# Optimization experiments

Measured on AMD Instinct MI355X. Metric: run time of the kernel, lower is better.

The kernel has to match this reference:

```python
import jax, jax.numpy as jnp
import numpy as np

N, K, P = 40000, 32, 15
C = 128            # output_feature_dim (kpconv in/out channels)
H_POS, D_POS = 64, 256
H_AGG, D_PROC = 256, 256
RADIUS = 1.0
KP_EXTENT = RADIUS / (P ** (1.0 / 3.0) - 1.0) * 1.5
SLOPE = 0.01       # nn.LeakyReLU default
EPS = 1e-5         # BatchNorm1d default eps


def _lin(key, din, dout):
    k1, k2 = jax.random.split(key)
    lim = 1.0 / np.sqrt(din)
    w = jax.random.uniform(k1, (din, dout), minval=-lim, maxval=lim, dtype=jnp.float32)
    b = jax.random.uniform(k2, (dout,), minval=-lim, maxval=lim, dtype=jnp.float32)
    return w, b


def _bn(x, g, b):
    # BatchNorm1d in training mode: biased batch statistics
    m = jnp.mean(x, axis=0)
    v = jnp.var(x, axis=0)
    return (x - m) * jax.lax.rsqrt(v + EPS) * g + b


def _lrelu(x):
    return jnp.where(x >= 0, x, SLOPE * x)


def setup_inputs() -> dict:
    key = jax.random.key(0)
    ks = jax.random.split(key, 16)
    inp = {}
    inp['points'] = jax.random.normal(ks[0], (N, 3), dtype=jnp.float32) * 10.0
    inp['covariances'] = jax.random.normal(ks[1], (N, 9), dtype=jnp.float32)
    inp['neighbors_index'] = jax.random.randint(ks[2], (N, K), 0, N)
    inp['pre_w'], inp['pre_b'] = _lin(ks[3], 9, C)
    inp['pre_bn_g'] = jnp.ones((C,), jnp.float32); inp['pre_bn_b'] = jnp.zeros((C,), jnp.float32)
    kp = jax.random.normal(ks[4], (P, 3), dtype=jnp.float32)
    kp = kp / jnp.linalg.norm(kp, axis=1, keepdims=True)
    inp['kernel_points'] = kp * jax.random.uniform(ks[5], (P, 1), dtype=jnp.float32) * RADIUS
    inp['kp_weights'] = jax.random.normal(ks[6], (P, C, C), dtype=jnp.float32) * (1.0 / np.sqrt(P * C))
    inp['pos_w1'], inp['pos_b1'] = _lin(ks[7], 3, H_POS)
    inp['pos_bn1_g'] = jnp.ones((H_POS,), jnp.float32); inp['pos_bn1_b'] = jnp.zeros((H_POS,), jnp.float32)
    inp['pos_w2'], inp['pos_b2'] = _lin(ks[8], H_POS, D_POS)
    inp['pos_bn2_g'] = jnp.ones((D_POS,), jnp.float32); inp['pos_bn2_b'] = jnp.zeros((D_POS,), jnp.float32)
    inp['agg_w1'], inp['agg_b1'] = _lin(ks[9], C, H_AGG)
    inp['agg_bn1_g'] = jnp.ones((H_AGG,), jnp.float32); inp['agg_bn1_b'] = jnp.zeros((H_AGG,), jnp.float32)
    inp['agg_w2'], inp['agg_b2'] = _lin(ks[10], H_AGG, D_PROC)
    inp['agg_bn2_g'] = jnp.ones((D_PROC,), jnp.float32); inp['agg_bn2_b'] = jnp.zeros((D_PROC,), jnp.float32)
    inp['keep_w1'], inp['keep_b1'] = _lin(ks[11], D_PROC, D_PROC // 4)
    inp['keep_bn_g'] = jnp.ones((D_PROC // 4,), jnp.float32); inp['keep_bn_b'] = jnp.zeros((D_PROC // 4,), jnp.float32)
    inp['keep_w2'], inp['keep_b2'] = _lin(ks[12], D_PROC // 4, 1)
    du = D_PROC + D_POS
    inp['uniq_w1'], inp['uniq_b1'] = _lin(ks[13], du, du // 4)
    inp['uniq_bn_g'] = jnp.ones((du // 4,), jnp.float32); inp['uniq_bn_b'] = jnp.zeros((du // 4,), jnp.float32)
    inp['uniq_w2'], inp['uniq_b2'] = _lin(ks[14], du // 4, 1)
    return inp


def reference(points, covariances, neighbors_index,
              pre_w, pre_b, pre_bn_g, pre_bn_b,
              kernel_points, kp_weights,
              pos_w1, pos_b1, pos_bn1_g, pos_bn1_b,
              pos_w2, pos_b2, pos_bn2_g, pos_bn2_b,
              agg_w1, agg_b1, agg_bn1_g, agg_bn1_b,
              agg_w2, agg_b2, agg_bn2_g, agg_bn2_b,
              keep_w1, keep_b1, keep_bn_g, keep_bn_b, keep_w2, keep_b2,
              uniq_w1, uniq_b1, uniq_bn_g, uniq_bn_b, uniq_w2, uniq_b2):
    # preactivation on 9-dim flattened covariances
    features = _lrelu(_bn(covariances @ pre_w + pre_b, pre_bn_g, pre_bn_b))  # [N, C]

    # ---- rigid KPConv (linear influence, sum aggregation, shadow point at index N) ----
    s_pad = jnp.concatenate([points, jnp.full((1, 3), 1e6, points.dtype)], axis=0)
    x_pad = jnp.concatenate([features, jnp.zeros((1, C), features.dtype)], axis=0)
    nb = s_pad[neighbors_index] - points[:, None, :]                          # [N, K, 3]
    # squared distances to kernel points without materializing [N,K,P,3]
    sq = (jnp.sum(nb * nb, -1)[:, :, None]
          + jnp.sum(kernel_points * kernel_points, -1)[None, None, :]
          - 2.0 * jnp.einsum('nkd,pd->nkp', nb, kernel_points))               # [N, K, P]
    infl = jnp.maximum(1.0 - jnp.sqrt(jnp.maximum(sq, 0.0)) / KP_EXTENT, 0.0)  # [N, K, P]
    nx = x_pad[neighbors_index]                                               # [N, K, C]
    weighted = jnp.einsum('nkp,nkc->npc', infl, nx)                           # [N, P, C]
    conv = jnp.einsum('npc,pcd->nd', weighted, kp_weights)                    # [N, C]
    # density normalization: count non-shadow neighbors
    nnum = jnp.maximum(jnp.sum(jnp.sum(nx, -1) > 0.0, axis=-1), 1)
    kpconv_feature = conv / nnum[:, None].astype(conv.dtype)

    # position embedding MLP
    pos = _lrelu(_bn(points @ pos_w1 + pos_b1, pos_bn1_g, pos_bn1_b))
    pos = _lrelu(_bn(pos @ pos_w2 + pos_b2, pos_bn2_g, pos_bn2_b))            # [N, 256]

    # feature aggregation MLP
    agg = _lrelu(_bn(kpconv_feature @ agg_w1 + agg_b1, agg_bn1_g, agg_bn1_b))
    agg = _lrelu(_bn(agg @ agg_w2 + agg_b2, agg_bn2_g, agg_bn2_b))            # [N, 256]

    # heads
    kh = _lrelu(_bn(agg @ keep_w1 + keep_b1, keep_bn_g, keep_bn_b))
    match_score = jax.nn.sigmoid((kh @ keep_w2 + keep_b2).ravel())
    u_in = jnp.concatenate([pos, agg], axis=1)                                # [N, 512]
    uh = _lrelu(_bn(u_in @ uniq_w1 + uniq_b1, uniq_bn_g, uniq_bn_b))
    unique_score = jax.nn.sigmoid((uh @ uniq_w2 + uniq_b2).ravel())
    return match_score, unique_score, neighbors_index
```

## Files before the change

### kernel.cpp

```cpp
#include <hip/hip_runtime.h>
#include <math.h>


#define NPTS 40000
#define KNB  32
#define PKP  15
#define SLOPE 0.01f
#define BNEPS 1e-5f
#define INV_N (1.0f/40000.0f)

typedef __attribute__((ext_vector_type(8))) short bf16x8;
typedef __attribute__((ext_vector_type(4))) float f32x4;

__device__ __forceinline__ float lrelu(float x){ return x >= 0.0f ? x : SLOPE*x; }
__device__ __forceinline__ unsigned short f2bf(float f){
  unsigned int b = __float_as_uint(f);
  b += 0x7fffu + ((b>>16)&1u);
  return (unsigned short)(b>>16);
}
__device__ __forceinline__ float bf2f(unsigned short u){
  return __uint_as_float(((unsigned int)u)<<16);
}


__global__ __launch_bounds__(256) void k_wprep_all(
    const float* __restrict__ kpw,  const float* __restrict__ pw2,
    const float* __restrict__ aw1,  const float* __restrict__ aw2,
    const float* __restrict__ kw1,  const float* __restrict__ uw1,
    unsigned short* __restrict__ wT){
  int i = blockIdx.x*256 + threadIdx.x;
  const float* src; int K, N, off, li;
  if      (i < 245760){ src=kpw; K=1920; N=128; off=0;      li=i; }
  else if (i < 262144){ src=pw2; K=64;   N=256; off=245760; li=i-245760; }
  else if (i < 294912){ src=aw1; K=128;  N=256; off=262144; li=i-262144; }
  else if (i < 360448){ src=aw2; K=256;  N=256; off=294912; li=i-294912; }
  else if (i < 376832){ src=kw1; K=256;  N=64;  off=360448; li=i-360448; }
  else                { src=uw1; K=512;  N=128; off=376832; li=i-376832; }
  int k = li / N, n = li - k*N;
  wT[(size_t)off + (size_t)n*K + k] = f2bf(src[li]);
}

__global__ __launch_bounds__(256) void k_moments(
    const float* __restrict__ cov, const float* __restrict__ pts,
    float* __restrict__ mom){
  int tid = threadIdx.x;
  int lane = tid & 63;
  int wv = (blockIdx.x*256 + tid) >> 6;
  int nw = gridDim.x*4;
  int kind = -1, ia = 0, ib = 0;
  if (lane < 9){ kind = 0; ia = lane; }
  else if (lane < 54){ int t = lane-9; int i = 0; while (t >= 9-i){ t -= 9-i; ++i; } kind = 1; ia = i; ib = i+t; }
  else if (lane < 57){ kind = 2; ia = lane-54; }
  else if (lane < 63){ int t = lane-57; int i = 0; while (t >= 3-i){ t -= 3-i; ++i; } kind = 3; ia = i; ib = i+t; }
  float part = 0.0f;
  for (int n = wv; n < NPTS; n += nw){
    float v = 0.0f;
    if (kind == 0) v = cov[n*9+ia];
    else if (kind == 1) v = cov[n*9+ia]*cov[n*9+ib];
    else if (kind == 2) v = pts[n*3+ia];
    else if (kind == 3) v = pts[n*3+ia]*pts[n*3+ib];
    part += v;
  }
  if (kind >= 0) atomicAdd(&mom[lane], part);
}

__global__ __launch_bounds__(256) void k_bnsetup(
    const float* __restrict__ preW, const float* __restrict__ preB,
    const float* __restrict__ preG, const float* __restrict__ preBB,
    const float* __restrict__ posW1, const float* __restrict__ posB1,
    const float* __restrict__ posG1, const float* __restrict__ posBB1,
    float* __restrict__ stats){
  int tid = threadIdx.x;
  const float* mom = stats + 2320;
  if (tid < 128){
    int c = tid;
    float wv[9];
    #pragma unroll
    for (int i = 0; i < 9; ++i) wv[i] = preW[i*128+c];
    float b = preB[c];
    float mw = 0.0f;
    #pragma unroll
    for (int i = 0; i < 9; ++i) mw += wv[i]*mom[i];
    mw *= INV_N;
    float quad = 0.0f;
    for (int i = 0; i < 9; ++i)
      for (int j = 0; j < 9; ++j){
        int ii = i < j ? i : j, jj = i < j ? j : i;
        quad += wv[i]*wv[j]*mom[9 + ii*9 - (ii*(ii-1))/2 + (jj-ii)];
      }
    quad *= INV_N;
    float mean = mw + b;
    float var = quad + 2.0f*b*mw + b*b - mean*mean;
    float sc = preG[c]*rsqrtf(var+BNEPS);
    stats[c]     = sc;
    stats[128+c] = preBB[c] - mean*sc + sc*b;
  } else if (tid < 192){
    int c = tid - 128;
    float w0 = posW1[c], w1 = posW1[64+c], w2 = posW1[128+c];
    float b = posB1[c];
    const float* pm = mom + 54;
    const float* pM = mom + 57;
    float mw = (w0*pm[0] + w1*pm[1] + w2*pm[2])*INV_N;
    float quad = (w0*w0*pM[0] + w1*w1*pM[3] + w2*w2*pM[5]
               + 2.0f*(w0*w1*pM[1] + w0*w2*pM[2] + w1*w2*pM[4]))*INV_N;
    float mean = mw + b;
    float var = quad + 2.0f*b*mw + b*b - mean*mean;
    float sc = posG1[c]*rsqrtf(var+BNEPS);
    stats[256+c] = sc;
    stats[320+c] = posBB1[c] - mean*sc + sc*b;
  }
}

__global__ __launch_bounds__(256) void k_feat(
    const float* __restrict__ cov, const float* __restrict__ preW,
    const float* __restrict__ stats, unsigned short* __restrict__ feat,
    float* __restrict__ fsum){
  int tid = threadIdx.x;
  int lane = tid & 63;
  int wv = (blockIdx.x*256 + tid) >> 6;
  int nw = gridDim.x*4;
  int c0 = lane, c1 = lane + 64;
  float w0[9], w1[9];
  #pragma unroll
  for (int i = 0; i < 9; ++i){ w0[i] = preW[i*128+c0]; w1[i] = preW[i*128+c1]; }
  float s0 = stats[c0], h0 = stats[128+c0];
  float s1 = stats[c1], h1 = stats[128+c1];
  for (int n = wv; n < NPTS; n += nw){
    float p0 = 0.0f, p1 = 0.0f;
    #pragma unroll
    for (int i = 0; i < 9; ++i){
      float x = cov[n*9+i];
      p0 += x*w0[i]; p1 += x*w1[i];
    }
    float f0 = lrelu(s0*p0 + h0);
    float f1 = lrelu(s1*p1 + h1);
    feat[(size_t)n*128 + c0] = f2bf(f0);
    feat[(size_t)n*128 + c1] = f2bf(f1);
    float t = f0 + f1;
    #pragma unroll
    for (int o = 32; o; o >>= 1) t += __shfl_down(t, o, 64);
    if (lane == 0) fsum[n] = t;
  }
}

__global__ __launch_bounds__(256) void k_scan(
    const float* __restrict__ pts, const int* __restrict__ nbr,
    const float* __restrict__ kp, const float* __restrict__ fsum,
    float* __restrict__ invn, int* __restrict__ list,
    int* __restrict__ gcount, float ext2){
  __shared__ float sKP[45];
  if (threadIdx.x < 45) sKP[threadIdx.x] = kp[threadIdx.x];
  __syncthreads();
  int wv   = (blockIdx.x*256 + threadIdx.x) >> 6;
  int lane = threadIdx.x & 63;
  int half = lane >> 5;
  int kk   = lane & 31;
  int n    = wv*2 + half;
  float px = pts[n*3+0], py = pts[n*3+1], pz = pts[n*3+2];
  int j = nbr[(size_t)n*KNB + kk];
  float nx = pts[j*3+0] - px;
  float ny = pts[j*3+1] - py;
  float nz = pts[j*3+2] - pz;
  float fs = fsum[j];
  bool anyp = false;
  #pragma unroll
  for (int p = 0; p < PKP; ++p){
    float dx = nx - sKP[p*3+0], dy = ny - sKP[p*3+1], dz = nz - sKP[p*3+2];
    anyp |= (dx*dx + dy*dy + dz*dz < ext2);
  }
  unsigned long long act  = __ballot(anyp);
  unsigned long long good = __ballot(fs > 0.0f);
  unsigned int actH  = half ? (unsigned int)(act  >> 32) : (unsigned int)act;
  unsigned int goodH = half ? (unsigned int)(good >> 32) : (unsigned int)good;
  if (kk == 0){
    int cnt = __popc(goodH);
    invn[n] = 1.0f / (float)(cnt < 1 ? 1 : cnt);
    if (actH){
      int pos = atomicAdd(gcount, 1);
      list[pos] = n;
    }
  }
}

__global__ __launch_bounds__(256) void k_conv_act(
    const float* __restrict__ pts, const int* __restrict__ nbr,
    const float* __restrict__ kp, const unsigned short* __restrict__ feat,
    const unsigned short* __restrict__ kpwT, const float* __restrict__ invn,
    const int* __restrict__ list, const int* __restrict__ gcount,
    unsigned short* __restrict__ kpfc, float ext2, float inv_ext){
  __shared__ float sW[PKP*128];
  __shared__ float sInfl[KNB*16];
  __shared__ unsigned int sPairP[KNB];
  __shared__ float sKP[45];
  __shared__ float sOut[128];
  __shared__ unsigned int sPmask, sPact;
  int tid = threadIdx.x;
  if (tid < 45) sKP[tid] = kp[tid];
  int cnt = *gcount;
  for (int it = blockIdx.x; it < cnt; it += gridDim.x){
    int n = list[it];
    if (tid == 0){ sPmask = 0u; sPact = 0u; }
    for (int i = tid; i < PKP*128; i += 256) sW[i] = 0.0f;
    __syncthreads();
    if (tid < KNB){
      int j = nbr[(size_t)n*KNB + tid];
      float nx = pts[j*3+0] - pts[n*3+0];
      float ny = pts[j*3+1] - pts[n*3+1];
      float nz = pts[j*3+2] - pts[n*3+2];
      unsigned int pm = 0u;
      #pragma unroll
      for (int p = 0; p < PKP; ++p){
        float dx = nx - sKP[p*3+0], dy = ny - sKP[p*3+1], dz = nz - sKP[p*3+2];
        float d2 = dx*dx + dy*dy + dz*dz;
        float infl = 0.0f;
        if (d2 < ext2){ infl = 1.0f - sqrtf(d2)*inv_ext; pm |= (1u << p); }
        sInfl[tid*16 + p] = infl;
      }
      sPairP[tid] = pm;
      if (pm){
        atomicOr(&sPact, 1u << tid);
        atomicOr(&sPmask, pm);
      }
    }
    __syncthreads();
    if (tid < 128){
      int c = tid;
      unsigned int m = sPact;
      while (m){
        int k = __ffs(m) - 1; m &= m - 1;
        int j = nbr[(size_t)n*KNB + k];
        float f = bf2f(feat[(size_t)j*128 + c]);
        unsigned int pp = sPairP[k];
        while (pp){
          int p = __ffs(pp) - 1; pp &= pp - 1;
          sW[p*128 + c] += sInfl[k*16 + p] * f;
        }
      }
    }
    __syncthreads();
    int d = tid & 127, h = tid >> 7;
    float acc = 0.0f;
    unsigned int pm = sPmask;
    while (pm){
      int p = __ffs(pm) - 1; pm &= pm - 1;
      const unsigned short* wp = kpwT + (size_t)d*1920 + p*128 + h*64;
      const float* wsrc = &sW[p*128 + h*64];
      #pragma unroll
      for (int c8 = 0; c8 < 8; ++c8){
        uint4 v = *(const uint4*)(wp + c8*8);
        unsigned int e[4] = {v.x, v.y, v.z, v.w};
        #pragma unroll
        for (int q = 0; q < 4; ++q){
          acc += wsrc[c8*8 + 2*q]     * bf2f((unsigned short)(e[q] & 0xffff));
          acc += wsrc[c8*8 + 2*q + 1] * bf2f((unsigned short)(e[q] >> 16));
        }
      }
    }
    if (h == 0) sOut[d] = acc;
    __syncthreads();
    if (h == 1) kpfc[(size_t)it*128 + d] = f2bf((sOut[d] + acc) * invn[n]);
    __syncthreads();
  }
}

__global__ __launch_bounds__(256) void k_posmom(
    const float* __restrict__ pts, const float* __restrict__ posW1,
    const float* __restrict__ stats, float* __restrict__ pm){
  __shared__ float sXm[64][65];
  int tid = threadIdx.x;
  int ia[9], ja[9];
  bool va[9];
  #pragma unroll
  for (int q = 0; q < 9; ++q){
    int idx = tid + q*256;
    va[q] = (idx < 2144);
    if (!va[q]){ ia[q] = 0; ja[q] = 0; continue; }
    if (idx < 64){ ia[q] = idx; ja[q] = -1; }
    else {
      int t = idx - 64; int i = 0;
      while (t >= 64 - i){ t -= 64 - i; ++i; }
      ia[q] = i; ja[q] = i + t;
    }
  }
  float acc[9] = {0,0,0,0,0,0,0,0,0};
  int c = tid & 63, rg = tid >> 6;
  float w0 = posW1[c], w1v = posW1[64+c], w2v = posW1[128+c];
  float sc1 = stats[256+c], sh1 = stats[320+c];
  for (int chunk = blockIdx.x; chunk < 625; chunk += gridDim.x){
    int base = chunk*64;
    for (int r = rg; r < 64; r += 4){
      int row = base + r;
      sXm[r][c] = lrelu(sc1*(pts[row*3+0]*w0 + pts[row*3+1]*w1v
                           + pts[row*3+2]*w2v) + sh1);
    }
    __syncthreads();
    #pragma unroll
    for (int q = 0; q < 9; ++q){
      if (!va[q]) continue;
      float a = 0.0f;
      if (ja[q] < 0){
        for (int r = 0; r < 64; ++r) a += sXm[r][ia[q]];
      } else {
        for (int r = 0; r < 64; ++r) a += sXm[r][ia[q]]*sXm[r][ja[q]];
      }
      acc[q] += a;
    }
    __syncthreads();
  }
  #pragma unroll
  for (int q = 0; q < 9; ++q)
    if (va[q]) atomicAdd(&pm[tid + q*256], acc[q]);
}

__global__ __launch_bounds__(256) void k_posbn2a(
    const float* __restrict__ pm, const float* __restrict__ posW2,
    float* __restrict__ U){
  __shared__ float sRow[64];
  int k = blockIdx.x;
  int tid = threadIdx.x;
  if (tid < 64){
    int i = k < tid ? k : tid, j = k < tid ? tid : k;
    int tri = i*64 - (i*(i-1))/2 + (j - i);
    sRow[tid] = pm[64 + tri];
  }
  __syncthreads();
  float a = 0.0f;
  for (int j = 0; j < 64; ++j) a += sRow[j]*posW2[j*256 + tid];
  U[k*256 + tid] = a;
}

__global__ __launch_bounds__(256) void k_posbn2b(
    const float* __restrict__ pm, const float* __restrict__ U,
    const float* __restrict__ posW2, const float* __restrict__ b2,
    const float* __restrict__ g2, const float* __restrict__ bb2,
    float* __restrict__ stats){
  int c = threadIdx.x;
  float mlin = 0.0f, quad = 0.0f;
  for (int k = 0; k < 64; ++k){
    float wkc = posW2[k*256 + c];
    mlin += wkc * pm[k];
    quad += wkc * U[k*256 + c];
  }
  mlin *= INV_N; quad *= INV_N;
  float b = b2[c];
  float mean = mlin + b;
  float var = quad + 2.0f*b*mlin + b*b - mean*mean;
  float sc = g2[c]*rsqrtf(var + BNEPS);
  stats[384+c] = sc;
  stats[640+c] = bb2[c] - mean*sc + sc*b;
}

__global__ __launch_bounds__(256) void k_ufused(
    const float* __restrict__ pts, const float* __restrict__ posW1,
    const float* __restrict__ stats, const unsigned short* __restrict__ posw2T,
    const unsigned short* __restrict__ uw1T, const float* __restrict__ ub_eff,
    unsigned short* __restrict__ u1, float* __restrict__ st2048){
  __shared__ __align__(16) unsigned short sX[4096];
  __shared__ __align__(16) unsigned short sY[16384];
  __shared__ float sC[512];
  __shared__ float sSum[128], sSq[128];
  int tid = threadIdx.x;
  int row0 = blockIdx.x*64;
  int w = tid >> 6, l = tid & 63;
  for (int i = tid; i < 512; i += 256) sC[i] = stats[384 + i];
  if (tid < 128){ sSum[tid] = 0.0f; sSq[tid] = 0.0f; }
  {
    int c = tid & 63, rg = tid >> 6;
    float w0 = posW1[c], w1v = posW1[64+c], w2v = posW1[128+c];
    float sc1 = stats[256+c], sh1 = stats[320+c];
    for (int r = rg; r < 64; r += 4){
      int row = row0 + r;
      float f = lrelu(sc1*(pts[row*3+0]*w0 + pts[row*3+1]*w1v
                         + pts[row*3+2]*w2v) + sh1);
      *(unsigned short*)((char*)sX + ((r*128 + c*2) ^ ((r&7)<<4))) = f2bf(f);
    }
  }
  __syncthreads();
  f32x4 acc1[16] = {};
  {
    int rowA = w*16 + (l & 15);
    #pragma unroll
    for (int m = 0; m < 2; ++m){
      int ka = m*32 + (l >> 4)*8;
      bf16x8 af = *(const bf16x8*)((const char*)sX + ((rowA*128 + ka*2) ^ ((rowA&7)<<4)));
      #pragma unroll
      for (int cf = 0; cf < 16; ++cf){
        int col = cf*16 + (l & 15);
        bf16x8 bfr = *(const bf16x8*)(posw2T + (size_t)col*64 + ka);
        acc1[cf] = __builtin_amdgcn_mfma_f32_16x16x32_bf16(af, bfr, acc1[cf], 0,0,0);
      }
    }
  }
  #pragma unroll
  for (int cf = 0; cf < 16; ++cf){
    int col = cf*16 + (l & 15);
    float sc = sC[col], sh = sC[256+col];
    #pragma unroll
    for (int r = 0; r < 4; ++r){
      int row = w*16 + (l >> 4)*4 + r;
      float y = lrelu(sc*acc1[cf][r] + sh);
      *(unsigned short*)((char*)sY + ((row*512 + col*2) ^ ((row&7)<<4))) = f2bf(y);
    }
  }
  __syncthreads();
  f32x4 acc2[8] = {};
  {
    int rowA = w*16 + (l & 15);
    #pragma unroll
    for (int m = 0; m < 8; ++m){
      int ka = m*32 + (l >> 4)*8;
      bf16x8 af = *(const bf16x8*)((const char*)sY + ((rowA*512 + ka*2) ^ ((rowA&7)<<4)));
      #pragma unroll
      for (int cf = 0; cf < 8; ++cf){
        int col = cf*16 + (l & 15);
        bf16x8 bfr = *(const bf16x8*)(uw1T + (size_t)col*512 + ka);
        acc2[cf] = __builtin_amdgcn_mfma_f32_16x16x32_bf16(af, bfr, acc2[cf], 0,0,0);
      }
    }
  }
  __syncthreads();
  #pragma unroll
  for (int cf = 0; cf < 8; ++cf){
    int col = cf*16 + (l & 15);
    float bj = ub_eff[col];
    float cs = 0.0f, cq = 0.0f;
    #pragma unroll
    for (int r = 0; r < 4; ++r){
      int row = w*16 + (l >> 4)*4 + r;
      float v = acc2[cf][r] + bj;
      sY[row*136 + col] = f2bf(v);
      cs += v; cq += v*v;
    }
    atomicAdd(&sSum[col], cs);
    atomicAdd(&sSq[col],  cq);
  }
  __syncthreads();
  #pragma unroll
  for (int ps = 0; ps < 4; ++ps){
    int idx = ps*256 + tid;
    int row = idx >> 4, c8 = idx & 15;
    uint4 v = *(const uint4*)(sY + row*136 + c8*8);
    *(uint4*)(u1 + (size_t)(row0+row)*128 + c8*8) = v;
  }
  if (tid < 128){
    atomicAdd(&st2048[tid],     sSum[tid]);
    atomicAdd(&st2048[128+tid], sSq[tid]);
  }
}

__global__ __launch_bounds__(256) void k_rowgemm(
    const unsigned short* __restrict__ X,
    const float* __restrict__ st, const float* __restrict__ g,
    const float* __restrict__ bb, int K, int norm,
    const unsigned short* __restrict__ Wt, const float* __restrict__ bias,
    int NOUT, unsigned short* __restrict__ Y, float* __restrict__ statsOut,
    const int* __restrict__ list, const int* __restrict__ gcount){
  __shared__ float xs[256];
  __shared__ float sSc[256], sSh[256];
  int tid = threadIdx.x;
  if (norm && tid < K){
    float s = st[tid], q = st[K+tid];
    float mean = s*INV_N, var = q*INV_N - mean*mean;
    float sc = g[tid]*rsqrtf(var+BNEPS);
    sSc[tid] = sc; sSh[tid] = bb[tid] - mean*sc;
  }
  __syncthreads();
  int cnt = *gcount;
  float rs = 0.0f, rq = 0.0f;
  for (int it = blockIdx.x; it < cnt; it += gridDim.x){
    if (tid < K){
      float xv = bf2f(X[(size_t)it*K + tid]);
      if (norm) xv = lrelu(xv*sSc[tid] + sSh[tid]);
      xs[tid] = xv;
    }
    __syncthreads();
    if (tid < NOUT){
      float acc = bias[tid];
      const unsigned short* wp = Wt + (size_t)tid*K;
      for (int k8 = 0; k8 < K; k8 += 8){
        uint4 v = *(const uint4*)(wp + k8);
        unsigned int e[4] = {v.x, v.y, v.z, v.w};
        #pragma unroll
        for (int q = 0; q < 4; ++q){
          acc += xs[k8+2*q]   * bf2f((unsigned short)(e[q] & 0xffff));
          acc += xs[k8+2*q+1] * bf2f((unsigned short)(e[q] >> 16));
        }
      }
      Y[(size_t)it*NOUT + tid] = f2bf(acc);
      rs += acc; rq += acc*acc;
    }
    __syncthreads();
  }
  if (tid < NOUT && rs != 0.0f){
    atomicAdd(&statsOut[tid],      rs);
    atomicAdd(&statsOut[NOUT+tid], rq);
  }
}

__global__ __launch_bounds__(256) void k_const1(
    const float* __restrict__ b1, const float* __restrict__ g1,
    const float* __restrict__ bb1, const unsigned short* __restrict__ aggw2T,
    const float* __restrict__ b2, float* __restrict__ st896,
    float* __restrict__ v2, const int* __restrict__ gcount){
  __shared__ float sX[256];
  int tid = threadIdx.x;
  float fN = (float)(NPTS - *gcount);
  float s = b1[tid];
  st896[tid]     += fN*s;
  st896[256+tid] += fN*s*s;
  float su = st896[tid], sq = st896[256+tid];
  float mean = su*INV_N, var = sq*INV_N - mean*mean;
  float sc = g1[tid]*rsqrtf(var+BNEPS);
  sX[tid] = lrelu(s*sc + bb1[tid] - mean*sc);
  __syncthreads();
  float acc = b2[tid];
  const unsigned short* wp = aggw2T + (size_t)tid*256;
  for (int k8 = 0; k8 < 256; k8 += 8){
    uint4 v = *(const uint4*)(wp + k8);
    unsigned int e[4] = {v.x, v.y, v.z, v.w};
    #pragma unroll
    for (int q = 0; q < 4; ++q){
      acc += sX[k8+2*q]   * bf2f((unsigned short)(e[q] & 0xffff));
      acc += sX[k8+2*q+1] * bf2f((unsigned short)(e[q] >> 16));
    }
  }
  v2[tid] = acc;
}

__global__ __launch_bounds__(256) void k_const2(
    const float* __restrict__ v2, const float* __restrict__ g2,
    const float* __restrict__ bb2, const unsigned short* __restrict__ keepw1T,
    const float* __restrict__ kb1, const unsigned short* __restrict__ uw1T,
    const float* __restrict__ ub1, float* __restrict__ st1408,
    float* __restrict__ v3, float* __restrict__ ub_eff,
    const int* __restrict__ gcount){
  __shared__ float sX[256];
  int tid = threadIdx.x;
  float fN = (float)(NPTS - *gcount);
  float s = v2[tid];
  st1408[tid]     += fN*s;
  st1408[256+tid] += fN*s*s;
  float su = st1408[tid], sq = st1408[256+tid];
  float mean = su*INV_N, var = sq*INV_N - mean*mean;
  float sc = g2[tid]*rsqrtf(var+BNEPS);
  sX[tid] = lrelu(s*sc + bb2[tid] - mean*sc);
  __syncthreads();
  if (tid < 64){
    float acc = kb1[tid];
    const unsigned short* wp = keepw1T + (size_t)tid*256;
    for (int k8 = 0; k8 < 256; k8 += 8){
      uint4 v = *(const uint4*)(wp + k8);
      unsigned int e[4] = {v.x, v.y, v.z, v.w};
      #pragma unroll
      for (int q = 0; q < 4; ++q){
        acc += sX[k8+2*q]   * bf2f((unsigned short)(e[q] & 0xffff));
        acc += sX[k8+2*q+1] * bf2f((unsigned short)(e[q] >> 16));
      }
    }
    v3[tid] = acc;
  } else if (tid < 192){
    int c = tid - 64;
    float acc = ub1[c];
    const unsigned short* wp = uw1T + (size_t)c*512 + 256;
    for (int k8 = 0; k8 < 256; k8 += 8){
      uint4 v = *(const uint4*)(wp + k8);
      unsigned int e[4] = {v.x, v.y, v.z, v.w};
      #pragma unroll
      for (int q = 0; q < 4; ++q){
        acc += sX[k8+2*q]   * bf2f((unsigned short)(e[q] & 0xffff));
        acc += sX[k8+2*q+1] * bf2f((unsigned short)(e[q] >> 16));
      }
    }
    ub_eff[c] = acc;
  }
}

__global__ __launch_bounds__(64) void k_const3(
    const float* __restrict__ v3, const float* __restrict__ g3,
    const float* __restrict__ bb3, const float* __restrict__ kw2,
    const float* __restrict__ kb2, float* __restrict__ st1920,
    float* __restrict__ s3out, const int* __restrict__ gcount){
  int tid = threadIdx.x;
  float fN = (float)(NPTS - *gcount);
  float s = v3[tid];
  st1920[tid]    += fN*s;
  st1920[64+tid] += fN*s*s;
  float su = st1920[tid], sq = st1920[64+tid];
  float mean = su*INV_N, var = sq*INV_N - mean*mean;
  float sc = g3[tid]*rsqrtf(var+BNEPS);
  float h = lrelu(s*sc + bb3[tid] - mean*sc) * kw2[tid];
  #pragma unroll
  for (int o = 32; o; o >>= 1) h += __shfl_down(h, o, 64);
  if (tid == 0) s3out[0] = 1.0f/(1.0f + expf(-(h + kb2[0])));
}

__global__ __launch_bounds__(256) void k_out(
    const int* __restrict__ nbr, const float* __restrict__ s3p,
    float* __restrict__ out){
  int i = blockIdx.x*256 + threadIdx.x;
  if (i < NPTS) out[i] = s3p[0];
  int4 v = ((const int4*)nbr)[i];
  ((float4*)(out + 2*NPTS))[i] =
      make_float4((float)v.x,(float)v.y,(float)v.z,(float)v.w);
}

__global__ __launch_bounds__(256) void k_keepact(
    const unsigned short* __restrict__ k1c, const float* __restrict__ st1920,
    const float* __restrict__ g3, const float* __restrict__ b3,
    const float* __restrict__ w2, const float* __restrict__ b2,
    float* __restrict__ out, const int* __restrict__ list,
    const int* __restrict__ gcount){
  int tid = threadIdx.x;
  int lane = tid & 63;
  int wv = (blockIdx.x*256 + tid) >> 6;
  int nw = gridDim.x*4;
  float su = st1920[lane], sq = st1920[64+lane];
  float mean = su*INV_N, var = sq*INV_N - mean*mean;
  float sc = g3[lane]*rsqrtf(var+BNEPS);
  float sh = b3[lane] - mean*sc;
  float w2v = w2[lane];
  int cnt = *gcount;
  for (int it = wv; it < cnt; it += nw){
    float h = lrelu(bf2f(k1c[(size_t)it*64 + lane])*sc + sh) * w2v;
    #pragma unroll
    for (int o = 32; o; o >>= 1) h += __shfl_down(h, o, 64);
    if (lane == 0) out[list[it]] = 1.0f/(1.0f + expf(-(h + b2[0])));
  }
}

__global__ __launch_bounds__(256) void k_udelta(
    const unsigned short* __restrict__ a2c, const float* __restrict__ st1408,
    const float* __restrict__ g2, const float* __restrict__ bb2,
    const unsigned short* __restrict__ uw1T, const float* __restrict__ ub1,
    const float* __restrict__ ub_eff, unsigned short* __restrict__ u1,
    float* __restrict__ st2048, const int* __restrict__ list,
    const int* __restrict__ gcount){
  __shared__ float sX[256];
  __shared__ float sSc[256], sSh[256];
  int tid = threadIdx.x;
  {
    float su = st1408[tid], sq = st1408[256+tid];
    float mean = su*INV_N, var = sq*INV_N - mean*mean;
    float sc = g2[tid]*rsqrtf(var+BNEPS);
    sSc[tid] = sc; sSh[tid] = bb2[tid] - mean*sc;
  }
  __syncthreads();
  int cnt = *gcount;
  for (int it = blockIdx.x; it < cnt; it += gridDim.x){
    int n = list[it];
    sX[tid] = lrelu(bf2f(a2c[(size_t)it*256 + tid])*sSc[tid] + sSh[tid]);
    __syncthreads();
    if (tid < 128){
      float acc = ub1[tid] - ub_eff[tid];
      const unsigned short* wp = uw1T + (size_t)tid*512 + 256;
      for (int k8 = 0; k8 < 256; k8 += 8){
        uint4 v = *(const uint4*)(wp + k8);
        unsigned int e[4] = {v.x, v.y, v.z, v.w};
        #pragma unroll
        for (int q = 0; q < 4; ++q){
          acc += sX[k8+2*q]   * bf2f((unsigned short)(e[q] & 0xffff));
          acc += sX[k8+2*q+1] * bf2f((unsigned short)(e[q] >> 16));
        }
      }
      float old = bf2f(u1[(size_t)n*128 + tid]);
      float neu = old + acc;
      u1[(size_t)n*128 + tid] = f2bf(neu);
      atomicAdd(&st2048[tid],     neu - old);
      atomicAdd(&st2048[128+tid], neu*neu - old*old);
    }
    __syncthreads();
  }
}

__global__ __launch_bounds__(256) void k_uhead(
    const unsigned short* __restrict__ u1, const float* __restrict__ st2048,
    const float* __restrict__ g, const float* __restrict__ b,
    const float* __restrict__ w2, const float* __restrict__ b2,
    float* __restrict__ out){
  __shared__ float sSc[128], sSh[128], sW2[128];
  int tid = threadIdx.x;
  if (tid < 128){
    float su = st2048[tid], sq = st2048[128+tid];
    float mean = su*INV_N, var = sq*INV_N - mean*mean;
    float sc = g[tid]*rsqrtf(var+BNEPS);
    sSc[tid] = sc; sSh[tid] = b[tid] - mean*sc;
    sW2[tid] = w2[tid];
  }
  __syncthreads();
  int lane = tid & 63, w = tid >> 6;
  int nw = gridDim.x*4;
  for (int n = blockIdx.x*4 + w; n < NPTS; n += nw){
    unsigned int v = *(const unsigned int*)(u1 + (size_t)n*128 + lane*2);
    int c0 = lane*2, c1 = c0 + 1;
    float h = lrelu(bf2f((unsigned short)(v & 0xffff))*sSc[c0] + sSh[c0])*sW2[c0]
            + lrelu(bf2f((unsigned short)(v >> 16))*sSc[c1] + sSh[c1])*sW2[c1];
    #pragma unroll
    for (int o = 32; o; o >>= 1) h += __shfl_down(h, o, 64);
    if (lane == 0) out[n] = 1.0f/(1.0f + expf(-(h + b2[0])));
  }
}

extern "C" void kernel_launch(void* const* d_in, const int* in_sizes, int n_in,
                              void* d_out, int out_size, void* d_ws, size_t ws_size,
                              hipStream_t stream) {
  const float* pts    = (const float*)d_in[0];
  const float* cov    = (const float*)d_in[1];
  const int*   nbr    = (const int*)  d_in[2];
  const float* pre_w  = (const float*)d_in[3];
  const float* pre_b  = (const float*)d_in[4];
  const float* pre_g  = (const float*)d_in[5];
  const float* pre_bb = (const float*)d_in[6];
  const float* kp     = (const float*)d_in[7];
  const float* kpw    = (const float*)d_in[8];
  const float* pos_w1 = (const float*)d_in[9];
  const float* pos_b1 = (const float*)d_in[10];
  const float* pos_g1 = (const float*)d_in[11];
  const float* pos_bb1= (const float*)d_in[12];
  const float* pos_w2 = (const float*)d_in[13];
  const float* pos_b2 = (const float*)d_in[14];
  const float* pos_g2 = (const float*)d_in[15];
  const float* pos_bb2= (const float*)d_in[16];
  const float* agg_w1 = (const float*)d_in[17];
  const float* agg_b1 = (const float*)d_in[18];
  const float* agg_g1 = (const float*)d_in[19];
  const float* agg_bb1= (const float*)d_in[20];
  const float* agg_w2 = (const float*)d_in[21];
  const float* agg_b2 = (const float*)d_in[22];
  const float* agg_g2 = (const float*)d_in[23];
  const float* agg_bb2= (const float*)d_in[24];
  const float* keep_w1= (const float*)d_in[25];
  const float* keep_b1= (const float*)d_in[26];
  const float* keep_g = (const float*)d_in[27];
  const float* keep_bb= (const float*)d_in[28];
  const float* keep_w2= (const float*)d_in[29];
  const float* keep_b2= (const float*)d_in[30];
  const float* uniq_w1= (const float*)d_in[31];
  const float* uniq_b1= (const float*)d_in[32];
  const float* uniq_g = (const float*)d_in[33];
  const float* uniq_bb= (const float*)d_in[34];
  const float* uniq_w2= (const float*)d_in[35];
  const float* uniq_b2= (const float*)d_in[36];

  float* out = (float*)d_out;

  char* wsb = (char*)d_ws;
  size_t off = 0;
  float* stats = (float*)(wsb + off); off += 8192*4;
  int*   gcount = (int*)(stats + 2304);
  float* s3     = stats + 2305;
  float* mom    = stats + 2320;
  float* v2     = stats + 2384;
  float* v3     = stats + 2640;
  float* ub_eff = stats + 2704;
  float* pm     = stats + 2832;
  float* U      = (float*)(wsb + off); off += 16384*4;
  unsigned short* wT = (unsigned short*)(wsb + off); off += (size_t)442368*2;
  unsigned short* kpwT   = wT;
  unsigned short* posw2T = wT + 245760;
  unsigned short* aggw1T = wT + 262144;
  unsigned short* aggw2T = wT + 294912;
  unsigned short* keepw1T= wT + 360448;
  unsigned short* uniqw1T= wT + 376832;
  float* fsum = (float*)(wsb + off); off += (size_t)NPTS*4;
  float* invn = (float*)(wsb + off); off += (size_t)NPTS*4;
  int*   list = (int*)  (wsb + off); off += (size_t)NPTS*4;
  unsigned short* feat = (unsigned short*)(wsb + off); off += (size_t)NPTS*128*2;
  unsigned short* kpfc = (unsigned short*)(wsb + off); off += (size_t)NPTS*128*2;
  unsigned short* a1c  = (unsigned short*)(wsb + off); off += (size_t)NPTS*256*2;
  unsigned short* a2c  = (unsigned short*)(wsb + off); off += (size_t)NPTS*256*2;
  unsigned short* k1c  = (unsigned short*)(wsb + off); off += (size_t)NPTS*64*2;
  unsigned short* u1   = (unsigned short*)(wsb + off); off += (size_t)NPTS*128*2;

  const double kpe = 1.0 / (cbrt(15.0) - 1.0) * 1.5;
  const float inv_ext = (float)(1.0 / kpe);
  const float ext2 = (float)(kpe * kpe);

  hipMemsetAsync(stats, 0, 4976*sizeof(float), stream);

  k_wprep_all<<<1728, 256, 0, stream>>>(kpw, pos_w2, agg_w1, agg_w2,
                                        keep_w1, uniq_w1, wT);
  k_moments<<<128, 256, 0, stream>>>(cov, pts, mom);
  k_bnsetup<<<1, 256, 0, stream>>>(pre_w, pre_b, pre_g, pre_bb,
                                   pos_w1, pos_b1, pos_g1, pos_bb1, stats);
  k_feat<<<2500, 256, 0, stream>>>(cov, pre_w, stats, feat, fsum);
  k_scan<<<5000, 256, 0, stream>>>(pts, nbr, kp, fsum, invn, list, gcount, ext2);
  k_conv_act<<<1024, 256, 0, stream>>>(pts, nbr, kp, feat, kpwT, invn,
                                       list, gcount, kpfc, ext2, inv_ext);

  k_posmom<<<160, 256, 0, stream>>>(pts, pos_w1, stats, pm);
  k_posbn2a<<<64, 256, 0, stream>>>(pm, pos_w2, U);
  k_posbn2b<<<1, 256, 0, stream>>>(pm, U, pos_w2, pos_b2, pos_g2, pos_bb2, stats);

  k_rowgemm<<<256, 256, 0, stream>>>(kpfc, nullptr, nullptr, nullptr, 128, 0,
                                     aggw1T, agg_b1, 256, a1c, stats + 896,
                                     list, gcount);
  k_const1<<<1, 256, 0, stream>>>(agg_b1, agg_g1, agg_bb1, aggw2T, agg_b2,
                                  stats + 896, v2, gcount);
  k_rowgemm<<<256, 256, 0, stream>>>(a1c, stats + 896, agg_g1, agg_bb1, 256, 1,
                                     aggw2T, agg_b2, 256, a2c, stats + 1408,
                                     list, gcount);
  k_const2<<<1, 256, 0, stream>>>(v2, agg_g2, agg_bb2, keepw1T, keep_b1,
                                  uniqw1T, uniq_b1, stats + 1408, v3, ub_eff,
                                  gcount);
  k_rowgemm<<<256, 256, 0, stream>>>(a2c, stats + 1408, agg_g2, agg_bb2, 256, 1,
                                     keepw1T, keep_b1, 64, k1c, stats + 1920,
                                     list, gcount);
  k_const3<<<1, 64, 0, stream>>>(v3, keep_g, keep_bb, keep_w2, keep_b2,
                                 stats + 1920, s3, gcount);

  k_out<<<1250, 256, 0, stream>>>(nbr, s3, out);
  k_keepact<<<32, 256, 0, stream>>>(k1c, stats + 1920, keep_g, keep_bb,
                                    keep_w2, keep_b2, out, list, gcount);

  k_ufused<<<625, 256, 0, stream>>>(pts, pos_w1, stats, posw2T, uniqw1T,
                                    ub_eff, u1, stats + 2048);
  k_udelta<<<128, 256, 0, stream>>>(a2c, stats + 1408, agg_g2, agg_bb2,
                                    uniqw1T, uniq_b1, ub_eff, u1, stats + 2048,
                                    list, gcount);
  k_uhead<<<2500, 256, 0, stream>>>(u1, stats + 2048, uniq_g, uniq_bb,
                                    uniq_w2, uniq_b2, out + NPTS);
}
```

Before: 309.9 us.

## Merge small kernels into combined launches and pre-swizzle MFMA B fragments

Merges weight prep and the moment reduction into one launch. The moments are now computed per row, reduced with wave shuffles and shared-memory atomics, and then added to global memory with atomics. It also merges the keep-head scatter into the u-delta kernel and the constant/neighbor output writes into the u-head kernel, removing three launches. It adds pos_w2 and uniq_w1 copies laid out in MFMA B-fragment order, so each lane in k_ufused reads 16 contiguous bytes instead of strided rows. The costs are extra branching inside the merged kernels and heavier register use in the moments path.

```diff
diff --git a/kernel.cpp b/kernel.cpp
--- a/kernel.cpp
+++ b/kernel.cpp
@@ -23,45 +23,80 @@
 }
 
 
-__global__ __launch_bounds__(256) void k_wprep_all(
+__global__ __launch_bounds__(256) void k_prep(
     const float* __restrict__ kpw,  const float* __restrict__ pw2,
     const float* __restrict__ aw1,  const float* __restrict__ aw2,
     const float* __restrict__ kw1,  const float* __restrict__ uw1,
-    unsigned short* __restrict__ wT){
-  int i = blockIdx.x*256 + threadIdx.x;
-  const float* src; int K, N, off, li;
-  if      (i < 245760){ src=kpw; K=1920; N=128; off=0;      li=i; }
-  else if (i < 262144){ src=pw2; K=64;   N=256; off=245760; li=i-245760; }
-  else if (i < 294912){ src=aw1; K=128;  N=256; off=262144; li=i-262144; }
-  else if (i < 360448){ src=aw2; K=256;  N=256; off=294912; li=i-294912; }
-  else if (i < 376832){ src=kw1; K=256;  N=64;  off=360448; li=i-360448; }
-  else                { src=uw1; K=512;  N=128; off=376832; li=i-376832; }
-  int k = li / N, n = li - k*N;
-  wT[(size_t)off + (size_t)n*K + k] = f2bf(src[li]);
-}
-
-__global__ __launch_bounds__(256) void k_moments(
+    unsigned short* __restrict__ wT,
+    unsigned short* __restrict__ posw2B, unsigned short* __restrict__ uw1B,
     const float* __restrict__ cov, const float* __restrict__ pts,
     float* __restrict__ mom){
-  int tid = threadIdx.x;
-  int lane = tid & 63;
-  int wv = (blockIdx.x*256 + tid) >> 6;
-  int nw = gridDim.x*4;
-  int kind = -1, ia = 0, ib = 0;
-  if (lane < 9){ kind = 0; ia = lane; }
-  else if (lane < 54){ int t = lane-9; int i = 0; while (t >= 9-i){ t -= 9-i; ++i; } kind = 1; ia = i; ib = i+t; }
-  else if (lane < 57){ kind = 2; ia = lane-54; }
-  else if (lane < 63){ int t = lane-57; int i = 0; while (t >= 3-i){ t -= 3-i; ++i; } kind = 3; ia = i; ib = i+t; }
-  float part = 0.0f;
-  for (int n = wv; n < NPTS; n += nw){
-    float v = 0.0f;
-    if (kind == 0) v = cov[n*9+ia];
-    else if (kind == 1) v = cov[n*9+ia]*cov[n*9+ib];
-    else if (kind == 2) v = pts[n*3+ia];
-    else if (kind == 3) v = pts[n*3+ia]*pts[n*3+ib];
-    part += v;
-  }
-  if (kind >= 0) atomicAdd(&mom[lane], part);
+  __shared__ float sM[63];
+  int bid = blockIdx.x, tid = threadIdx.x;
+  if (bid < 1728){
+    int i = bid*256 + tid;
+    const float* src; int K, N, off, li;
+    if      (i < 245760){ src=kpw; K=1920; N=128; off=0;      li=i; }
+    else if (i < 262144){ src=pw2; K=64;   N=256; off=245760; li=i-245760; }
+    else if (i < 294912){ src=aw1; K=128;  N=256; off=262144; li=i-262144; }
+    else if (i < 360448){ src=aw2; K=256;  N=256; off=294912; li=i-294912; }
+    else if (i < 376832){ src=kw1; K=256;  N=64;  off=360448; li=i-360448; }
+    else                { src=uw1; K=512;  N=128; off=376832; li=i-376832; }
+    int k = li / N, n = li - k*N;
+    wT[(size_t)off + (size_t)n*K + k] = f2bf(src[li]);
+  } else if (bid < 1920){
+    int i2 = (bid-1728)*256 + tid;
+    if (i2 < 16384){
+      int f = i2 >> 9, l = (i2 >> 3) & 63, j = i2 & 7;
+      int cf = f >> 1, m = f & 1;
+      int k = m*32 + (l>>4)*8 + j;
+      int col = cf*16 + (l & 15);
+      posw2B[i2] = f2bf(pw2[k*256 + col]);
+    } else {
+      int i3 = i2 - 16384;
+      int f = i3 >> 9, l = (i3 >> 3) & 63, j = i3 & 7;
+      int cf = f >> 3, m = f & 7;
+      int k = m*32 + (l>>4)*8 + j;
+      int c = cf*16 + (l & 15);
+      uw1B[i3] = f2bf(uw1[k*128 + c]);
+    }
+  } else {
+    int lane = tid & 63;
+    int row = (bid-1920)*256 + tid;
+    if (tid < 63) sM[tid] = 0.0f;
+    __syncthreads();
+    float c9[9] = {0,0,0,0,0,0,0,0,0};
+    float p3[3] = {0,0,0};
+    if (row < NPTS){
+      #pragma unroll
+      for (int i = 0; i < 9; ++i) c9[i] = cov[row*9+i];
+      #pragma unroll
+      for (int i = 0; i < 3; ++i) p3[i] = pts[row*3+i];
+    }
+    float vals[63];
+    int q = 0;
+    #pragma unroll
+    for (int i = 0; i < 9; ++i) vals[q++] = c9[i];
+    #pragma unroll
+    for (int i = 0; i < 9; ++i)
+      #pragma unroll
+      for (int j = i; j < 9; ++j) vals[q++] = c9[i]*c9[j];
+    #pragma unroll
+    for (int i = 0; i < 3; ++i) vals[q++] = p3[i];
+    #pragma unroll
+    for (int i = 0; i < 3; ++i)
+      #pragma unroll
+      for (int j = i; j < 3; ++j) vals[q++] = p3[i]*p3[j];
+    #pragma unroll
+    for (int qq = 0; qq < 63; ++qq){
+      float v = vals[qq];
+      #pragma unroll
+      for (int o = 32; o; o >>= 1) v += __shfl_down(v, o, 64);
+      if (lane == 0) atomicAdd(&sM[qq], v);
+    }
+    __syncthreads();
+    if (tid < 63) atomicAdd(&mom[tid], sM[tid]);
+  }
 }
 
 __global__ __launch_bounds__(256) void k_bnsetup(
@@ -352,8 +387,8 @@
 
 __global__ __launch_bounds__(256) void k_ufused(
     const float* __restrict__ pts, const float* __restrict__ posW1,
-    const float* __restrict__ stats, const unsigned short* __restrict__ posw2T,
-    const unsigned short* __restrict__ uw1T, const float* __restrict__ ub_eff,
+    const float* __restrict__ stats, const unsigned short* __restrict__ posw2B,
+    const unsigned short* __restrict__ uw1B, const float* __restrict__ ub_eff,
     unsigned short* __restrict__ u1, float* __restrict__ st2048){
   __shared__ __align__(16) unsigned short sX[4096];
   __shared__ __align__(16) unsigned short sY[16384];
@@ -385,8 +420,7 @@
       bf16x8 af = *(const bf16x8*)((const char*)sX + ((rowA*128 + ka*2) ^ ((rowA&7)<<4)));
       #pragma unroll
       for (int cf = 0; cf < 16; ++cf){
-        int col = cf*16 + (l & 15);
-        bf16x8 bfr = *(const bf16x8*)(posw2T + (size_t)col*64 + ka);
+        bf16x8 bfr = *(const bf16x8*)(posw2B + (size_t)(cf*2+m)*512 + l*8);
         acc1[cf] = __builtin_amdgcn_mfma_f32_16x16x32_bf16(af, bfr, acc1[cf], 0,0,0);
       }
     }
@@ -412,8 +446,7 @@
       bf16x8 af = *(const bf16x8*)((const char*)sY + ((rowA*512 + ka*2) ^ ((rowA&7)<<4)));
       #pragma unroll
       for (int cf = 0; cf < 8; ++cf){
-        int col = cf*16 + (l & 15);
-        bf16x8 bfr = *(const bf16x8*)(uw1T + (size_t)col*512 + ka);
+        bf16x8 bfr = *(const bf16x8*)(uw1B + (size_t)(cf*8+m)*512 + l*8);
         acc2[cf] = __builtin_amdgcn_mfma_f32_16x16x32_bf16(af, bfr, acc2[cf], 0,0,0);
       }
     }
@@ -594,91 +627,86 @@
   if (tid == 0) s3out[0] = 1.0f/(1.0f + expf(-(h + kb2[0])));
 }
 
-__global__ __launch_bounds__(256) void k_out(
-    const int* __restrict__ nbr, const float* __restrict__ s3p,
-    float* __restrict__ out){
-  int i = blockIdx.x*256 + threadIdx.x;
-  if (i < NPTS) out[i] = s3p[0];
-  int4 v = ((const int4*)nbr)[i];
-  ((float4*)(out + 2*NPTS))[i] =
-      make_float4((float)v.x,(float)v.y,(float)v.z,(float)v.w);
-}
-
-__global__ __launch_bounds__(256) void k_keepact(
-    const unsigned short* __restrict__ k1c, const float* __restrict__ st1920,
-    const float* __restrict__ g3, const float* __restrict__ b3,
-    const float* __restrict__ w2, const float* __restrict__ b2,
-    float* __restrict__ out, const int* __restrict__ list,
-    const int* __restrict__ gcount){
-  int tid = threadIdx.x;
-  int lane = tid & 63;
-  int wv = (blockIdx.x*256 + tid) >> 6;
-  int nw = gridDim.x*4;
-  float su = st1920[lane], sq = st1920[64+lane];
-  float mean = su*INV_N, var = sq*INV_N - mean*mean;
-  float sc = g3[lane]*rsqrtf(var+BNEPS);
-  float sh = b3[lane] - mean*sc;
-  float w2v = w2[lane];
-  int cnt = *gcount;
-  for (int it = wv; it < cnt; it += nw){
-    float h = lrelu(bf2f(k1c[(size_t)it*64 + lane])*sc + sh) * w2v;
-    #pragma unroll
-    for (int o = 32; o; o >>= 1) h += __shfl_down(h, o, 64);
-    if (lane == 0) out[list[it]] = 1.0f/(1.0f + expf(-(h + b2[0])));
-  }
-}
-
-__global__ __launch_bounds__(256) void k_udelta(
+__global__ __launch_bounds__(256) void k_udelta_keep(
     const unsigned short* __restrict__ a2c, const float* __restrict__ st1408,
     const float* __restrict__ g2, const float* __restrict__ bb2,
     const unsigned short* __restrict__ uw1T, const float* __restrict__ ub1,
     const float* __restrict__ ub_eff, unsigned short* __restrict__ u1,
-    float* __restrict__ st2048, const int* __restrict__ list,
-    const int* __restrict__ gcount){
+    float* __restrict__ st2048,
+    const unsigned short* __restrict__ k1c, const float* __restrict__ st1920,
+    const float* __restrict__ g3, const float* __restrict__ b3,
+    const float* __restrict__ kw2, const float* __restrict__ kb2,
+    float* __restrict__ out,
+    const int* __restrict__ list, const int* __restrict__ gcount){
   __shared__ float sX[256];
   __shared__ float sSc[256], sSh[256];
   int tid = threadIdx.x;
-  {
-    float su = st1408[tid], sq = st1408[256+tid];
+  int cnt = *gcount;
+  if (blockIdx.x < 128){
+    {
+      float su = st1408[tid], sq = st1408[256+tid];
+      float mean = su*INV_N, var = sq*INV_N - mean*mean;
+      float sc = g2[tid]*rsqrtf(var+BNEPS);
+      sSc[tid] = sc; sSh[tid] = bb2[tid] - mean*sc;
+    }
+    __syncthreads();
+    for (int it = blockIdx.x; it < cnt; it += 128){
+      int n = list[it];
+      sX[tid] = lrelu(bf2f(a2c[(size_t)it*256 + tid])*sSc[tid] + sSh[tid]);
+      __syncthreads();
+      if (tid < 128){
+        float acc = ub1[tid] - ub_eff[tid];
+        const unsigned short* wp = uw1T + (size_t)tid*512 + 256;
+        for (int k8 = 0; k8 < 256; k8 += 8){
+          uint4 v = *(const uint4*)(wp + k8);
+          unsigned int e[4] = {v.x, v.y, v.z, v.w};
+          #pragma unroll
+          for (int q = 0; q < 4; ++q){
+            acc += sX[k8+2*q]   * bf2f((unsigned short)(e[q] & 0xffff));
+            acc += sX[k8+2*q+1] * bf2f((unsigned short)(e[q] >> 16));
+          }
+        }
+        float old = bf2f(u1[(size_t)n*128 + tid]);
+        float neu = old + acc;
+        u1[(size_t)n*128 + tid] = f2bf(neu);
+        atomicAdd(&st2048[tid],     neu - old);
+        atomicAdd(&st2048[128+tid], neu*neu - old*old);
+      }
+      __syncthreads();
+    }
+  } else {
+    int lane = tid & 63;
+    int wv = (blockIdx.x - 128)*4 + (tid >> 6);
+    float su = st1920[lane], sq = st1920[64+lane];
     float mean = su*INV_N, var = sq*INV_N - mean*mean;
-    float sc = g2[tid]*rsqrtf(var+BNEPS);
-    sSc[tid] = sc; sSh[tid] = bb2[tid] - mean*sc;
-  }
-  __syncthreads();
-  int cnt = *gcount;
-  for (int it = blockIdx.x; it < cnt; it += gridDim.x){
-    int n = list[it];
-    sX[tid] = lrelu(bf2f(a2c[(size_t)it*256 + tid])*sSc[tid] + sSh[tid]);
-    __syncthreads();
-    if (tid < 128){
-      float acc = ub1[tid] - ub_eff[tid];
-      const unsigned short* wp = uw1T + (size_t)tid*512 + 256;
-      for (int k8 = 0; k8 < 256; k8 += 8){
-        uint4 v = *(const uint4*)(wp + k8);
-        unsigned int e[4] = {v.x, v.y, v.z, v.w};
-        #pragma unroll
-        for (int q = 0; q < 4; ++q){
-          acc += sX[k8+2*q]   * bf2f((unsigned short)(e[q] & 0xffff));
-          acc += sX[k8+2*q+1] * bf2f((unsigned short)(e[q] >> 16));
-        }
-      }
-      float old = bf2f(u1[(size_t)n*128 + tid]);
-      float neu = old + acc;
-      u1[(size_t)n*128 + tid] = f2bf(neu);
-      atomicAdd(&st2048[tid],     neu - old);
-      atomicAdd(&st2048[128+tid], neu*neu - old*old);
-    }
-    __syncthreads();
-  }
-}
-
-__global__ __launch_bounds__(256) void k_uhead(
+    float sc = g3[lane]*rsqrtf(var+BNEPS);
+    float sh = b3[lane] - mean*sc;
+    float w2v = kw2[lane];
+    for (int it = wv; it < cnt; it += 128){
+      float h = lrelu(bf2f(k1c[(size_t)it*64 + lane])*sc + sh) * w2v;
+      #pragma unroll
+      for (int o = 32; o; o >>= 1) h += __shfl_down(h, o, 64);
+      if (lane == 0) out[list[it]] = 1.0f/(1.0f + expf(-(h + kb2[0])));
+    }
+  }
+}
+
+__global__ __launch_bounds__(256) void k_uhead_out(
     const unsigned short* __restrict__ u1, const float* __restrict__ st2048,
     const float* __restrict__ g, const float* __restrict__ b,
     const float* __restrict__ w2, const float* __restrict__ b2,
+    const int* __restrict__ nbr, const float* __restrict__ s3p,
     float* __restrict__ out){
   __shared__ float sSc[128], sSh[128], sW2[128];
   int tid = threadIdx.x;
+  if (blockIdx.x >= 2500){
+    int i = (blockIdx.x - 2500)*256 + tid;
+    if (i < NPTS) out[i] = s3p[0];
+    int4 v = ((const int4*)nbr)[i];
+    ((float4*)(out + 2*NPTS))[i] =
+        make_float4((float)v.x,(float)v.y,(float)v.z,(float)v.w);
+    return;
+  }
   if (tid < 128){
     float su = st2048[tid], sq = st2048[128+tid];
     float mean = su*INV_N, var = sq*INV_N - mean*mean;
@@ -688,15 +716,14 @@
   }
   __syncthreads();
   int lane = tid & 63, w = tid >> 6;
-  int nw = gridDim.x*4;
-  for (int n = blockIdx.x*4 + w; n < NPTS; n += nw){
+  for (int n = blockIdx.x*4 + w; n < NPTS; n += 10000){
     unsigned int v = *(const unsigned int*)(u1 + (size_t)n*128 + lane*2);
     int c0 = lane*2, c1 = c0 + 1;
     float h = lrelu(bf2f((unsigned short)(v & 0xffff))*sSc[c0] + sSh[c0])*sW2[c0]
             + lrelu(bf2f((unsigned short)(v >> 16))*sSc[c1] + sSh[c1])*sW2[c1];
     #pragma unroll
     for (int o = 32; o; o >>= 1) h += __shfl_down(h, o, 64);
-    if (lane == 0) out[n] = 1.0f/(1.0f + expf(-(h + b2[0])));
+    if (lane == 0) out[NPTS + n] = 1.0f/(1.0f + expf(-(h + b2[0])));
   }
 }
 
@@ -756,11 +783,12 @@
   float* U      = (float*)(wsb + off); off += 16384*4;
   unsigned short* wT = (unsigned short*)(wsb + off); off += (size_t)442368*2;
   unsigned short* kpwT   = wT;
-  unsigned short* posw2T = wT + 245760;
   unsigned short* aggw1T = wT + 262144;
   unsigned short* aggw2T = wT + 294912;
   unsigned short* keepw1T= wT + 360448;
   unsigned short* uniqw1T= wT + 376832;
+  unsigned short* posw2B = (unsigned short*)(wsb + off); off += (size_t)16384*2;
+  unsigned short* uw1B   = (unsigned short*)(wsb + off); off += (size_t)32768*2;
   float* fsum = (float*)(wsb + off); off += (size_t)NPTS*4;
   float* invn = (float*)(wsb + off); off += (size_t)NPTS*4;
   int*   list = (int*)  (wsb + off); off += (size_t)NPTS*4;
@@ -777,9 +805,8 @@
 
   hipMemsetAsync(stats, 0, 4976*sizeof(float), stream);
 
-  k_wprep_all<<<1728, 256, 0, stream>>>(kpw, pos_w2, agg_w1, agg_w2,
-                                        keep_w1, uniq_w1, wT);
-  k_moments<<<128, 256, 0, stream>>>(cov, pts, mom);
+  k_prep<<<2080, 256, 0, stream>>>(kpw, pos_w2, agg_w1, agg_w2, keep_w1,
+                                   uniq_w1, wT, posw2B, uw1B, cov, pts, mom);
   k_bnsetup<<<1, 256, 0, stream>>>(pre_w, pre_b, pre_g, pre_bb,
                                    pos_w1, pos_b1, pos_g1, pos_bb1, stats);
   k_feat<<<2500, 256, 0, stream>>>(cov, pre_w, stats, feat, fsum);
@@ -808,15 +835,13 @@
   k_const3<<<1, 64, 0, stream>>>(v3, keep_g, keep_bb, keep_w2, keep_b2,
                                  stats + 1920, s3, gcount);
 
-  k_out<<<1250, 256, 0, stream>>>(nbr, s3, out);
-  k_keepact<<<32, 256, 0, stream>>>(k1c, stats + 1920, keep_g, keep_bb,
-                                    keep_w2, keep_b2, out, list, gcount);
-
-  k_ufused<<<625, 256, 0, stream>>>(pts, pos_w1, stats, posw2T, uniqw1T,
+  k_ufused<<<625, 256, 0, stream>>>(pts, pos_w1, stats, posw2B, uw1B,
                                     ub_eff, u1, stats + 2048);
-  k_udelta<<<128, 256, 0, stream>>>(a2c, stats + 1408, agg_g2, agg_bb2,
-                                    uniqw1T, uniq_b1, ub_eff, u1, stats + 2048,
-                                    list, gcount);
-  k_uhead<<<2500, 256, 0, stream>>>(u1, stats + 2048, uniq_g, uniq_bb,
-                                    uniq_w2, uniq_b2, out + NPTS);
-}
+  k_udelta_keep<<<160, 256, 0, stream>>>(a2c, stats + 1408, agg_g2, agg_bb2,
+                                         uniqw1T, uniq_b1, ub_eff, u1,
+                                         stats + 2048, k1c, stats + 1920,
+                                         keep_g, keep_bb, keep_w2, keep_b2,
+                                         out, list, gcount);
+  k_uhead_out<<<3750, 256, 0, stream>>>(u1, stats + 2048, uniq_g, uniq_bb,
+                                        uniq_w2, uniq_b2, nbr, s3, out);
+}
```

Measured after the change: 277.5 us. -10.5%, faster.
